# Optimization experiments

Measured on AMD Instinct MI355X. Metric: run time of the kernel, lower is better.

Reference implementation:

```python
import jax, jax.numpy as jnp
import numpy as np

B, S, D, M = 4, 2048, 1024, 4  # batch, seq_len, d_model, n_stride_masks


def setup_inputs() -> dict:
    key = jax.random.key(0)
    ks = jax.random.split(key, 10)
    lin = lambda k: jax.random.normal(k, (D, D), jnp.float32) / np.float32(np.sqrt(D))
    return {
        "x": jax.random.normal(ks[0], (B, S, D), jnp.float32),
        "stride_masks": jax.random.randint(ks[1], (M, S, S), 0, 2, jnp.int32),
        "Wq": lin(ks[2]), "bq": jnp.zeros((D,), jnp.float32),
        "Wk": lin(ks[3]), "bk": jnp.zeros((D,), jnp.float32),
        "Wv": lin(ks[4]), "bv": jnp.zeros((D,), jnp.float32),
        "Wo": lin(ks[5]), "bo": jnp.zeros((D,), jnp.float32),
    }


def reference(x, stride_masks, Wq, bq, Wk, bk, Wv, bv, Wo, bo):
    scale = jnp.float32(np.sqrt(D))
    Q = x @ Wq + bq  # [B,S,D]
    K = x @ Wk + bk
    V = x @ Wv + bv
    # scores are identical for every mask; compute once (same math as the loop)
    scores = jnp.einsum("bqd,bkd->bqk", Q, K) / scale  # [B,S,S]
    masked = jnp.where(stride_masks[:, None] == 0, jnp.float32(-1e9), scores[None])  # [M,B,S,S]
    weights = jax.nn.softmax(masked, axis=-1)
    # sum over masks then divide by M == mean(stack(outs), 0)
    out = jnp.einsum("mbqk,bkd->bqd", weights, V) / jnp.float32(M)
    return out @ Wo + bo
```

## Files before the change

kernel.cpp:

```cpp
#include <hip/hip_runtime.h>
#include <hip/hip_bf16.h>
#include <stdint.h>

#define B_ 4
#define S_ 2048
#define D_ 1024
#define M_ 4

typedef __bf16 bf16;
typedef _Float16 f16;
typedef unsigned char u8;
typedef __bf16 bf16x8 __attribute__((ext_vector_type(8)));
typedef _Float16 f16x8 __attribute__((ext_vector_type(8)));
typedef float f32x4 __attribute__((ext_vector_type(4)));

__device__ __forceinline__ void async_copy16(const void* g, void* l) {
  __builtin_amdgcn_global_load_lds(
      (const __attribute__((address_space(1))) void*)g,
      (__attribute__((address_space(3))) void*)l, 16, 0, 0);
}

__global__ __launch_bounds__(256) void prep(
    const float* __restrict__ x, const float* __restrict__ w0,
    const float* __restrict__ w1, const float* __restrict__ w2,
    const float* __restrict__ w3, const int* __restrict__ masks,
    bf16* __restrict__ xc, bf16* __restrict__ WT, u8* __restrict__ pk) {
  __shared__ bf16 t[64][65];
  const int blk = blockIdx.x;
  const int tid = threadIdx.x;
  const long SS = (long)S_ * S_;

  if (blk < 4096) {
    const long i = (long)blk * 2048 + tid * 8;
    const float4 a = *(const float4*)(x + i);
    const float4 b = *(const float4*)(x + i + 4);
    bf16x8 o;
    o[0] = (bf16)a.x; o[1] = (bf16)a.y; o[2] = (bf16)a.z; o[3] = (bf16)a.w;
    o[4] = (bf16)b.x; o[5] = (bf16)b.y; o[6] = (bf16)b.z; o[7] = (bf16)b.w;
    *(bf16x8*)(xc + i) = o;
  } else if (blk < 5120) {
    const int local = blk - 4096;
    const int z = local >> 8;
    const int rem = local & 255;
    const int r0 = (rem >> 4) * 64;
    const int c0 = (rem & 15) * 64;
    const int tx = tid & 63;
    const int ty = tid >> 6;
    const float* in = (z == 0) ? w0 : (z == 1) ? w1 : (z == 2) ? w2 : w3;
    bf16* out = WT + (long)z * D_ * D_;
    for (int i = ty; i < 64; i += 4)
      t[i][tx] = (bf16)in[(long)(r0 + i) * D_ + c0 + tx];
    __syncthreads();
    for (int i = ty; i < 64; i += 4)
      out[(long)(c0 + i) * D_ + r0 + tx] = t[tx][i];
  } else {
    const long e = (long)(blk - 5120) * 2048 + tid * 8;
    unsigned long long wv = 0;
#pragma unroll
    for (int m = 0; m < M_; ++m) {
      const int4 a = *(const int4*)(masks + m * SS + e);
      const int4 b = *(const int4*)(masks + m * SS + e + 4);
      const int v[8] = {a.x, a.y, a.z, a.w, b.x, b.y, b.z, b.w};
#pragma unroll
      for (int j = 0; j < 8; ++j)
        wv |= (unsigned long long)(v[j] != 0 ? 1u : 0u) << (8 * j + m);
    }
    *(unsigned long long*)(pk + e) = wv;
  }
}

__global__ __launch_bounds__(256) void transposeB(
    const bf16* __restrict__ in, bf16* __restrict__ out,
    int rows, int cols, long ib, long ob) {
  __shared__ bf16 t[64][65];
  in += (long)blockIdx.z * ib;
  out += (long)blockIdx.z * ob;
  const int r0 = blockIdx.y * 64;
  const int c0 = blockIdx.x * 64;
  const int tx = threadIdx.x & 63;
  const int ty = threadIdx.x >> 6;
#pragma unroll
  for (int i = ty; i < 64; i += 4) t[i][tx] = in[(long)(r0 + i) * cols + c0 + tx];
  __syncthreads();
#pragma unroll
  for (int i = ty; i < 64; i += 4) out[(long)(c0 + i) * rows + r0 + tx] = t[tx][i];
}

#define MODE_PLAIN 0
#define MODE_EXP 1
#define MODE_QKV 2

template <typename OutT, int MODE>
__global__ __launch_bounds__(256) void gemm_bt(
    const bf16* __restrict__ A, long aB, int lda,
    const bf16* __restrict__ Bt, long bB, int ldb,
    OutT* __restrict__ C, long cB, int ldc,
    const float* __restrict__ bias0, const float* __restrict__ bias1,
    const float* __restrict__ bias2, float alpha, int K) {
  __shared__ __align__(16) bf16 As[2][128 * 64];
  __shared__ __align__(16) bf16 Bs[2][128 * 64];
  const int tid = threadIdx.x;
  const int lane = tid & 63;
  const int w = tid >> 6;
  const int wm = w & 1;
  const int wn = w >> 1;
  A += (long)blockIdx.z * aB;
  Bt += (long)blockIdx.z * bB;
  if (MODE != MODE_QKV) C += (long)blockIdx.z * cB;

  const int gx = gridDim.x;
  const int pid = blockIdx.y * gx + blockIdx.x;
  const int gsz = 16 * gx;
  const int bym = (pid / gsz) * 16 + (pid % 16);
  const int bxm = (pid % gsz) / 16;

  const int row0 = bym * 128;
  const int col0 = bxm * 128;
  const int quad = lane >> 4;
  const int l15 = lane & 15;
  const int srow = lane >> 3;
  const int scol = (lane & 7) * 8;

  f32x4 acc[4][4];
#pragma unroll
  for (int i = 0; i < 4; ++i)
#pragma unroll
    for (int j = 0; j < 4; ++j) acc[i][j] = (f32x4){0.f, 0.f, 0.f, 0.f};

  const int nk = K >> 6;

#pragma unroll
  for (int c = 0; c < 4; ++c) {
    const int r = c * 32 + w * 8;
    async_copy16(A + (long)(row0 + r + srow) * lda + scol, &As[0][r * 64]);
    async_copy16(Bt + (long)(col0 + r + srow) * ldb + scol, &Bs[0][r * 64]);
  }

  for (int i = 0; i < nk; ++i) {
    const int cur = i & 1;
    __syncthreads();
    if (i + 1 < nk) {
      const int kt = (i + 1) << 6;
      const int nxt = cur ^ 1;
#pragma unroll
      for (int c = 0; c < 4; ++c) {
        const int r = c * 32 + w * 8;
        async_copy16(A + (long)(row0 + r + srow) * lda + kt + scol, &As[nxt][r * 64]);
        async_copy16(Bt + (long)(col0 + r + srow) * ldb + kt + scol, &Bs[nxt][r * 64]);
      }
    }
#pragma unroll
    for (int ks = 0; ks < 2; ++ks) {
      bf16x8 af[4], bf[4];
#pragma unroll
      for (int j = 0; j < 4; ++j) {
        af[j] = *(const bf16x8*)&As[cur][(wm * 64 + j * 16 + l15) * 64 + ks * 32 + quad * 8];
        bf[j] = *(const bf16x8*)&Bs[cur][(wn * 64 + j * 16 + l15) * 64 + ks * 32 + quad * 8];
      }
#pragma unroll
      for (int mi = 0; mi < 4; ++mi)
#pragma unroll
        for (int ni = 0; ni < 4; ++ni)
          acc[mi][ni] = __builtin_amdgcn_mfma_f32_16x16x32_bf16(af[mi], bf[ni], acc[mi][ni], 0, 0, 0);
    }
  }

  const int grp = (MODE == MODE_QKV) ? (bxm >> 3) : 0;
  const float* bias = (MODE == MODE_QKV)
                          ? (grp == 0 ? bias0 : grp == 1 ? bias1 : bias2)
                          : bias0;
  const long NX = (long)B_ * S_ * D_;

#pragma unroll
  for (int mi = 0; mi < 4; ++mi)
#pragma unroll
    for (int ni = 0; ni < 4; ++ni) {
      const int col = col0 + wn * 64 + ni * 16 + l15;
      const int lcol = col & (D_ - 1);
      const float bv = bias ? bias[MODE == MODE_QKV ? lcol : col] : 0.0f;
#pragma unroll
      for (int r = 0; r < 4; ++r) {
        const int row = row0 + wm * 64 + mi * 16 + quad * 4 + r;
        const float val = acc[mi][ni][r] * alpha + bv;
        if (MODE == MODE_EXP) {
          C[(long)row * ldc + col] = (OutT)__expf(val);
        } else if (MODE == MODE_QKV) {
          C[grp * NX + (long)row * D_ + lcol] = (OutT)val;
        } else {
          C[(long)row * ldc + col] = (OutT)val;
        }
      }
    }
}

__device__ __forceinline__ void stage_half(const bf16* __restrict__ G, int ld,
                                           int row_base, int kcol,
                                           bf16* region, int tid) {
  const int r = tid >> 2;
  const int c = ((tid & 3) ^ ((tid >> 3) & 3)) << 3;
  const bf16* g = G + (long)(row_base + r) * ld + kcol + c;
  bf16* dst = region + ((tid >> 6) << 9);
  async_copy16(g, dst);
  async_copy16(g + (long)128 * ld, dst + 4096);
}

template <typename OutT, int MODE>
__global__ __launch_bounds__(512) void gemm256(
    const bf16* __restrict__ A, long aB, int lda,
    const bf16* __restrict__ Bt, long bB, int ldb,
    OutT* __restrict__ C, long cB, int ldc,
    const float* __restrict__ bias0, const float* __restrict__ bias1,
    const float* __restrict__ bias2, float alpha, int K) {
  __shared__ __align__(16) bf16 As[2][2][256 * 32];
  __shared__ __align__(16) bf16 Bs[2][2][256 * 32];
  const int tid = threadIdx.x;
  const int lane = tid & 63;
  const int w = tid >> 6;
  const int wm = w & 1;
  const int wn = w >> 1;
  const int quad = lane >> 4;
  const int l15 = lane & 15;
  const int fse = (quad ^ ((l15 >> 1) & 3)) << 3;

  A += (long)blockIdx.z * aB;
  Bt += (long)blockIdx.z * bB;
  if (MODE != MODE_QKV) C += (long)blockIdx.z * cB;

  const int gx = gridDim.x;
  const int pid = blockIdx.y * gx + blockIdx.x;
  const int gsz = 8 * gx;
  const int bym = (pid / gsz) * 8 + (pid % 8);
  const int bxm = (pid % gsz) / 8;
  const int row0 = bym * 256;
  const int col0 = bxm * 256;

  f32x4 acc[8][4];
#pragma unroll
  for (int i = 0; i < 8; ++i)
#pragma unroll
    for (int j = 0; j < 4; ++j) acc[i][j] = (f32x4){0.f, 0.f, 0.f, 0.f};

  const int nk = K >> 6;

  stage_half(A, lda, row0, 0, &As[0][0][0], tid);
  stage_half(Bt, ldb, col0, 0, &Bs[0][0][0], tid);
  stage_half(A, lda, row0, 32, &As[0][1][0], tid);
  stage_half(Bt, ldb, col0, 32, &Bs[0][1][0], tid);
  if (nk > 1) {
    stage_half(A, lda, row0, 64, &As[1][0][0], tid);
    stage_half(Bt, ldb, col0, 64, &Bs[1][0][0], tid);
    asm volatile("s_waitcnt vmcnt(4)" ::: "memory");
  } else {
    asm volatile("s_waitcnt vmcnt(0)" ::: "memory");
  }
  __builtin_amdgcn_s_barrier();
  __builtin_amdgcn_sched_barrier(0);

  for (int t = 0; t < nk; ++t) {
    const int buf = t & 1;
    bf16x8 af[8], b0, b1;

#pragma unroll
    for (int m = 0; m < 8; ++m)
      af[m] = *(const bf16x8*)&As[buf][0][(wm * 128 + m * 16 + l15) * 32 + fse];
    b0 = *(const bf16x8*)&Bs[buf][0][(wn * 64 + l15) * 32 + fse];
    b1 = *(const bf16x8*)&Bs[buf][0][(wn * 64 + 16 + l15) * 32 + fse];
    if (t + 1 < nk)
      stage_half(A, lda, row0, ((t + 1) << 6) + 32, &As[buf ^ 1][1][0], tid);
    __builtin_amdgcn_s_setprio(1);
#pragma unroll
    for (int m = 0; m < 8; ++m) {
      acc[m][0] = __builtin_amdgcn_mfma_f32_16x16x32_bf16(af[m], b0, acc[m][0], 0, 0, 0);
      acc[m][1] = __builtin_amdgcn_mfma_f32_16x16x32_bf16(af[m], b1, acc[m][1], 0, 0, 0);
    }
    __builtin_amdgcn_s_setprio(0);
    __builtin_amdgcn_s_barrier();
    __builtin_amdgcn_sched_barrier(0);

    b0 = *(const bf16x8*)&Bs[buf][0][(wn * 64 + 32 + l15) * 32 + fse];
    b1 = *(const bf16x8*)&Bs[buf][0][(wn * 64 + 48 + l15) * 32 + fse];
    if (t + 1 < nk)
      stage_half(Bt, ldb, col0, ((t + 1) << 6) + 32, &Bs[buf ^ 1][1][0], tid);
    __builtin_amdgcn_s_setprio(1);
#pragma unroll
    for (int m = 0; m < 8; ++m) {
      acc[m][2] = __builtin_amdgcn_mfma_f32_16x16x32_bf16(af[m], b0, acc[m][2], 0, 0, 0);
      acc[m][3] = __builtin_amdgcn_mfma_f32_16x16x32_bf16(af[m], b1, acc[m][3], 0, 0, 0);
    }
    __builtin_amdgcn_s_setprio(0);
    __builtin_amdgcn_s_barrier();
    __builtin_amdgcn_sched_barrier(0);

#pragma unroll
    for (int m = 0; m < 8; ++m)
      af[m] = *(const bf16x8*)&As[buf][1][(wm * 128 + m * 16 + l15) * 32 + fse];
    b0 = *(const bf16x8*)&Bs[buf][1][(wn * 64 + l15) * 32 + fse];
    b1 = *(const bf16x8*)&Bs[buf][1][(wn * 64 + 16 + l15) * 32 + fse];
    if (t + 2 < nk)
      stage_half(A, lda, row0, (t + 2) << 6, &As[buf][0][0], tid);
    __builtin_amdgcn_s_setprio(1);
#pragma unroll
    for (int m = 0; m < 8; ++m) {
      acc[m][0] = __builtin_amdgcn_mfma_f32_16x16x32_bf16(af[m], b0, acc[m][0], 0, 0, 0);
      acc[m][1] = __builtin_amdgcn_mfma_f32_16x16x32_bf16(af[m], b1, acc[m][1], 0, 0, 0);
    }
    __builtin_amdgcn_s_setprio(0);
    __builtin_amdgcn_s_barrier();
    __builtin_amdgcn_sched_barrier(0);

    b0 = *(const bf16x8*)&Bs[buf][1][(wn * 64 + 32 + l15) * 32 + fse];
    b1 = *(const bf16x8*)&Bs[buf][1][(wn * 64 + 48 + l15) * 32 + fse];
    if (t + 2 < nk)
      stage_half(Bt, ldb, col0, (t + 2) << 6, &Bs[buf][0][0], tid);
    if (t + 2 < nk)
      asm volatile("s_waitcnt vmcnt(4)" ::: "memory");
    else
      asm volatile("s_waitcnt vmcnt(0)" ::: "memory");
    __builtin_amdgcn_s_setprio(1);
#pragma unroll
    for (int m = 0; m < 8; ++m) {
      acc[m][2] = __builtin_amdgcn_mfma_f32_16x16x32_bf16(af[m], b0, acc[m][2], 0, 0, 0);
      acc[m][3] = __builtin_amdgcn_mfma_f32_16x16x32_bf16(af[m], b1, acc[m][3], 0, 0, 0);
    }
    __builtin_amdgcn_s_setprio(0);
    __builtin_amdgcn_s_barrier();
    __builtin_amdgcn_sched_barrier(0);
  }

  const int grp = (MODE == MODE_QKV) ? (bxm >> 2) : 0;
  const float* bias = (MODE == MODE_QKV)
                          ? (grp == 0 ? bias0 : grp == 1 ? bias1 : bias2)
                          : bias0;
  const long NX = (long)B_ * S_ * D_;
#pragma unroll
  for (int mi = 0; mi < 8; ++mi)
#pragma unroll
    for (int ni = 0; ni < 4; ++ni) {
      const int col = col0 + wn * 64 + ni * 16 + l15;
      const int lcol = col & (D_ - 1);
      const float bv = bias ? bias[MODE == MODE_QKV ? lcol : col] : 0.0f;
#pragma unroll
      for (int r = 0; r < 4; ++r) {
        const int row = row0 + wm * 128 + mi * 16 + quad * 4 + r;
        const float val = acc[mi][ni][r] * alpha + bv;
        if (MODE == MODE_EXP) {
          C[(long)row * ldc + col] = (OutT)__expf(val);
        } else if (MODE == MODE_QKV) {
          C[grp * NX + (long)row * D_ + lcol] = (OutT)val;
        } else {
          C[(long)row * ldc + col] = (OutT)val;
        }
      }
    }
}

__global__ __launch_bounds__(256) void softmax_combine(
    const f16* __restrict__ E, const u8* __restrict__ pk, bf16* __restrict__ P) {
  const int q = blockIdx.x;
  const int b = blockIdx.y;
  const int tid = threadIdx.x;
  const int lane = tid & 63;
  const int wv = tid >> 6;
  __shared__ float4 red[4];

  float e[8];
  {
    const f16x8 h = *(const f16x8*)(E + ((long)b * S_ + q) * S_ + tid * 8);
#pragma unroll
    for (int j = 0; j < 8; ++j) e[j] = (float)h[j];
  }
  const unsigned long long mb =
      *(const unsigned long long*)(pk + (long)q * S_ + tid * 8);

  float4 s = {0.f, 0.f, 0.f, 0.f};
#pragma unroll
  for (int j = 0; j < 8; ++j) {
    const unsigned bits = (unsigned)(mb >> (8 * j)) & 0xF;
    const float ev = e[j];
    if (bits & 1) s.x += ev;
    if (bits & 2) s.y += ev;
    if (bits & 4) s.z += ev;
    if (bits & 8) s.w += ev;
  }
#pragma unroll
  for (int o = 32; o > 0; o >>= 1) {
    s.x += __shfl_xor(s.x, o, 64);
    s.y += __shfl_xor(s.y, o, 64);
    s.z += __shfl_xor(s.z, o, 64);
    s.w += __shfl_xor(s.w, o, 64);
  }
  if (lane == 0) red[wv] = s;
  __syncthreads();
  const float4 t0 = red[0], t1 = red[1], t2 = red[2], t3 = red[3];
  const float r0 = 0.25f / (t0.x + t1.x + t2.x + t3.x);
  const float r1 = 0.25f / (t0.y + t1.y + t2.y + t3.y);
  const float r2 = 0.25f / (t0.z + t1.z + t2.z + t3.z);
  const float r3 = 0.25f / (t0.w + t1.w + t2.w + t3.w);

  bf16x8 o;
#pragma unroll
  for (int j = 0; j < 8; ++j) {
    const unsigned bits = (unsigned)(mb >> (8 * j)) & 0xF;
    const float wgt = ((bits & 1) ? r0 : 0.f) + ((bits & 2) ? r1 : 0.f) +
                      ((bits & 4) ? r2 : 0.f) + ((bits & 8) ? r3 : 0.f);
    o[j] = (bf16)(e[j] * wgt);
  }
  *(bf16x8*)(P + ((long)b * S_ + q) * S_ + tid * 8) = o;
}

extern "C" void kernel_launch(void* const* d_in, const int* in_sizes, int n_in,
                              void* d_out, int out_size, void* d_ws, size_t ws_size,
                              hipStream_t stream) {
  const float* x = (const float*)d_in[0];
  const int* masks = (const int*)d_in[1];
  const float* bq = (const float*)d_in[3];
  const float* bk = (const float*)d_in[5];
  const float* bv = (const float*)d_in[7];
  const float* bo = (const float*)d_in[9];
  float* out = (float*)d_out;

  const long DD = (long)D_ * D_;
  const long SD = (long)S_ * D_;
  const long NX = (long)B_ * SD;
  const long SS = (long)S_ * S_;

  bf16* xc = (bf16*)d_ws;
  bf16* WqT = xc + NX;
  bf16* WoT = WqT + 3 * DD;
  u8* pk = (u8*)(WoT + DD);
  bf16* Q = (bf16*)(pk + SS);
  bf16* K = Q + NX;
  bf16* V = K + NX;
  bf16* VT = V + NX;
  bf16* P = VT + NX;
  f16* E = (f16*)(P + (long)B_ * SS);
  bf16* attn = Q;

  dim3 blk(256);
  dim3 blk512(512);

  prep<<<dim3(7168), blk, 0, stream>>>(
      x, (const float*)d_in[2], (const float*)d_in[4], (const float*)d_in[6],
      (const float*)d_in[8], masks, xc, WqT, pk);

  gemm256<bf16, MODE_QKV><<<dim3(12, 32), blk512, 0, stream>>>(
      xc, 0, D_, WqT, 0, D_, Q, 0, D_, bq, bk, bv, 1.0f, D_);

  transposeB<<<dim3(16, 32, B_), blk, 0, stream>>>(V, VT, S_, D_, SD, SD);

  gemm256<f16, MODE_EXP><<<dim3(8, 8, B_), blk512, 0, stream>>>(
      Q, SD, D_, K, SD, D_, E, SS, S_, nullptr, nullptr, nullptr, 1.0f / 32.0f, D_);

  softmax_combine<<<dim3(S_, B_), blk, 0, stream>>>(E, pk, P);

  gemm_bt<bf16, MODE_PLAIN><<<dim3(8, 16, B_), blk, 0, stream>>>(
      P, SS, S_, VT, SD, S_, attn, SD, D_, nullptr, nullptr, nullptr, 1.0f, S_);

  gemm_bt<float, MODE_PLAIN><<<dim3(8, 64), blk, 0, stream>>>(
      attn, 0, D_, WoT, 0, D_, out, 0, D_, bo, nullptr, nullptr, 1.0f, D_);
}
```

Before: 370.8 us.

## Replace gemm_bt with 256x128 half-K pipelined gemmA for QKV, PV and output projections

Adds a new 512-thread GEMM kernel with 256x128 tiles that splits each 64-wide K step into two 32-wide halves. Each half is staged asynchronously into swizzled LDS buffers under explicit vmcnt waits, raw barriers and raised wave priority around the MFMA block. It replaces the 128x128 gemm_bt used for P@V and the output projection, and the gemm256 used for the QKV projection. The aim is to overlap global loads with MFMA work and avoid LDS bank conflicts, at the cost of hand-counted waitcnt logic that must match the number of issued copies exactly.

```diff
diff --git a/kernel.cpp b/kernel.cpp
--- a/kernel.cpp
+++ b/kernel.cpp
@@ -89,37 +89,61 @@
 #define MODE_PLAIN 0
 #define MODE_EXP 1
 #define MODE_QKV 2
+#define MODE_PV 3
+
+__device__ __forceinline__ void stage128(const bf16* __restrict__ G, int ld,
+                                         int kcol, bf16* region, int tid) {
+  const int r = tid >> 2;
+  const int c = ((tid & 3) ^ ((tid >> 3) & 3)) << 3;
+  async_copy16(G + (long)r * ld + kcol + c, region + ((tid >> 6) << 9));
+}
+__device__ __forceinline__ void stage256(const bf16* __restrict__ G, int ld,
+                                         int kcol, bf16* region, int tid) {
+  const int r = tid >> 2;
+  const int c = ((tid & 3) ^ ((tid >> 3) & 3)) << 3;
+  const bf16* g = G + (long)r * ld + kcol + c;
+  bf16* dst = region + ((tid >> 6) << 9);
+  async_copy16(g, dst);
+  async_copy16(g + (long)128 * ld, dst + 4096);
+}
 
 template <typename OutT, int MODE>
-__global__ __launch_bounds__(256) void gemm_bt(
-    const bf16* __restrict__ A, long aB, int lda,
-    const bf16* __restrict__ Bt, long bB, int ldb,
-    OutT* __restrict__ C, long cB, int ldc,
+__global__ __launch_bounds__(512) void gemmA(
+    const bf16* __restrict__ A, int lda,
+    const bf16* __restrict__ Bt, long bzs, int ldb,
+    OutT* __restrict__ C, int ldc,
     const float* __restrict__ bias0, const float* __restrict__ bias1,
     const float* __restrict__ bias2, float alpha, int K) {
-  __shared__ __align__(16) bf16 As[2][128 * 64];
-  __shared__ __align__(16) bf16 Bs[2][128 * 64];
+  __shared__ __align__(16) bf16 As[2][2][256 * 32];
+  __shared__ __align__(16) bf16 Bs[2][2][128 * 32];
   const int tid = threadIdx.x;
   const int lane = tid & 63;
   const int w = tid >> 6;
-  const int wm = w & 1;
-  const int wn = w >> 1;
-  A += (long)blockIdx.z * aB;
-  Bt += (long)blockIdx.z * bB;
-  if (MODE != MODE_QKV) C += (long)blockIdx.z * cB;
+  const int wm = w & 3;
+  const int wn = w >> 2;
+  const int quad = lane >> 4;
+  const int l15 = lane & 15;
+  const int fse = (quad ^ ((l15 >> 1) & 3)) << 3;
 
   const int gx = gridDim.x;
   const int pid = blockIdx.y * gx + blockIdx.x;
-  const int gsz = 16 * gx;
-  const int bym = (pid / gsz) * 16 + (pid % 16);
-  const int bxm = (pid % gsz) / 16;
-
-  const int row0 = bym * 128;
+  const int gsz = 8 * gx;
+  const int bym = (pid / gsz) * 8 + (pid % 8);
+  const int bxm = (pid % gsz) / 8;
+  const int row0 = bym * 256;
   const int col0 = bxm * 128;
-  const int quad = lane >> 4;
-  const int l15 = lane & 15;
-  const int srow = lane >> 3;
-  const int scol = (lane & 7) * 8;
+
+  const bf16* Arow = A + (long)row0 * lda;
+  const bf16* Bcol;
+  int grp = 0;
+  if (MODE == MODE_QKV) {
+    grp = col0 >> 10;
+    Bcol = Bt + (long)grp * ((long)D_ * D_) + (long)(col0 & (D_ - 1)) * ldb;
+  } else if (MODE == MODE_PV) {
+    Bcol = Bt + (long)(row0 >> 11) * bzs + (long)col0 * ldb;
+  } else {
+    Bcol = Bt + (long)col0 * ldb;
+  }
 
   f32x4 acc[4][4];
 #pragma unroll
@@ -129,65 +153,89 @@
 
   const int nk = K >> 6;
 
-#pragma unroll
-  for (int c = 0; c < 4; ++c) {
-    const int r = c * 32 + w * 8;
-    async_copy16(A + (long)(row0 + r + srow) * lda + scol, &As[0][r * 64]);
-    async_copy16(Bt + (long)(col0 + r + srow) * ldb + scol, &Bs[0][r * 64]);
-  }
-
-  for (int i = 0; i < nk; ++i) {
-    const int cur = i & 1;
-    __syncthreads();
-    if (i + 1 < nk) {
-      const int kt = (i + 1) << 6;
-      const int nxt = cur ^ 1;
-#pragma unroll
-      for (int c = 0; c < 4; ++c) {
-        const int r = c * 32 + w * 8;
-        async_copy16(A + (long)(row0 + r + srow) * lda + kt + scol, &As[nxt][r * 64]);
-        async_copy16(Bt + (long)(col0 + r + srow) * ldb + kt + scol, &Bs[nxt][r * 64]);
-      }
-    }
-#pragma unroll
-    for (int ks = 0; ks < 2; ++ks) {
-      bf16x8 af[4], bf[4];
-#pragma unroll
-      for (int j = 0; j < 4; ++j) {
-        af[j] = *(const bf16x8*)&As[cur][(wm * 64 + j * 16 + l15) * 64 + ks * 32 + quad * 8];
-        bf[j] = *(const bf16x8*)&Bs[cur][(wn * 64 + j * 16 + l15) * 64 + ks * 32 + quad * 8];
-      }
-#pragma unroll
-      for (int mi = 0; mi < 4; ++mi)
-#pragma unroll
-        for (int ni = 0; ni < 4; ++ni)
-          acc[mi][ni] = __builtin_amdgcn_mfma_f32_16x16x32_bf16(af[mi], bf[ni], acc[mi][ni], 0, 0, 0);
-    }
-  }
-
-  const int grp = (MODE == MODE_QKV) ? (bxm >> 3) : 0;
+  stage256(Arow, lda, 0, &As[0][0][0], tid);
+  stage128(Bcol, ldb, 0, &Bs[0][0][0], tid);
+  stage256(Arow, lda, 32, &As[0][1][0], tid);
+  stage128(Bcol, ldb, 32, &Bs[0][1][0], tid);
+  stage256(Arow, lda, 64, &As[1][0][0], tid);
+  stage128(Bcol, ldb, 64, &Bs[1][0][0], tid);
+  asm volatile("s_waitcnt vmcnt(3)" ::: "memory");
+  __builtin_amdgcn_s_barrier();
+  __builtin_amdgcn_sched_barrier(0);
+
+  for (int t = 0; t < nk; ++t) {
+    const int buf = t & 1;
+    bf16x8 af[4], bf[4];
+
+#pragma unroll
+    for (int j = 0; j < 4; ++j) {
+      af[j] = *(const bf16x8*)&As[buf][0][(wm * 64 + j * 16 + l15) * 32 + fse];
+      bf[j] = *(const bf16x8*)&Bs[buf][0][(wn * 64 + j * 16 + l15) * 32 + fse];
+    }
+    if (t + 1 < nk) {
+      const int kt = ((t + 1) << 6) + 32;
+      stage256(Arow, lda, kt, &As[buf ^ 1][1][0], tid);
+      stage128(Bcol, ldb, kt, &Bs[buf ^ 1][1][0], tid);
+    }
+    __builtin_amdgcn_s_setprio(1);
+#pragma unroll
+    for (int mi = 0; mi < 4; ++mi)
+#pragma unroll
+      for (int ni = 0; ni < 4; ++ni)
+        acc[mi][ni] = __builtin_amdgcn_mfma_f32_16x16x32_bf16(af[mi], bf[ni], acc[mi][ni], 0, 0, 0);
+    __builtin_amdgcn_s_setprio(0);
+    if (t + 1 < nk)
+      asm volatile("s_waitcnt vmcnt(6)" ::: "memory");
+    else
+      asm volatile("s_waitcnt vmcnt(0)" ::: "memory");
+    __builtin_amdgcn_s_barrier();
+    __builtin_amdgcn_sched_barrier(0);
+
+#pragma unroll
+    for (int j = 0; j < 4; ++j) {
+      af[j] = *(const bf16x8*)&As[buf][1][(wm * 64 + j * 16 + l15) * 32 + fse];
+      bf[j] = *(const bf16x8*)&Bs[buf][1][(wn * 64 + j * 16 + l15) * 32 + fse];
+    }
+    if (t + 2 < nk) {
+      const int kt = (t + 2) << 6;
+      stage256(Arow, lda, kt, &As[buf][0][0], tid);
+      stage128(Bcol, ldb, kt, &Bs[buf][0][0], tid);
+    }
+    __builtin_amdgcn_s_setprio(1);
+#pragma unroll
+    for (int mi = 0; mi < 4; ++mi)
+#pragma unroll
+      for (int ni = 0; ni < 4; ++ni)
+        acc[mi][ni] = __builtin_amdgcn_mfma_f32_16x16x32_bf16(af[mi], bf[ni], acc[mi][ni], 0, 0, 0);
+    __builtin_amdgcn_s_setprio(0);
+    if (t + 2 < nk)
+      asm volatile("s_waitcnt vmcnt(6)" ::: "memory");
+    else if (t + 1 < nk)
+      asm volatile("s_waitcnt vmcnt(3)" ::: "memory");
+    __builtin_amdgcn_s_barrier();
+    __builtin_amdgcn_sched_barrier(0);
+  }
+
   const float* bias = (MODE == MODE_QKV)
                           ? (grp == 0 ? bias0 : grp == 1 ? bias1 : bias2)
                           : bias0;
   const long NX = (long)B_ * S_ * D_;
-
+  OutT* Cb = (MODE == MODE_QKV) ? C + (long)grp * NX : C;
 #pragma unroll
   for (int mi = 0; mi < 4; ++mi)
 #pragma unroll
     for (int ni = 0; ni < 4; ++ni) {
       const int col = col0 + wn * 64 + ni * 16 + l15;
-      const int lcol = col & (D_ - 1);
-      const float bv = bias ? bias[MODE == MODE_QKV ? lcol : col] : 0.0f;
+      const int ccol = (MODE == MODE_QKV) ? (col & (D_ - 1)) : col;
+      const float bv = bias ? bias[ccol] : 0.0f;
 #pragma unroll
       for (int r = 0; r < 4; ++r) {
         const int row = row0 + wm * 64 + mi * 16 + quad * 4 + r;
         const float val = acc[mi][ni][r] * alpha + bv;
-        if (MODE == MODE_EXP) {
-          C[(long)row * ldc + col] = (OutT)__expf(val);
-        } else if (MODE == MODE_QKV) {
-          C[grp * NX + (long)row * D_ + lcol] = (OutT)val;
+        if (MODE == MODE_QKV) {
+          Cb[(long)row * D_ + ccol] = (OutT)val;
         } else {
-          C[(long)row * ldc + col] = (OutT)val;
+          Cb[(long)row * ldc + col] = (OutT)val;
         }
       }
     }
@@ -443,8 +491,8 @@
       x, (const float*)d_in[2], (const float*)d_in[4], (const float*)d_in[6],
       (const float*)d_in[8], masks, xc, WqT, pk);
 
-  gemm256<bf16, MODE_QKV><<<dim3(12, 32), blk512, 0, stream>>>(
-      xc, 0, D_, WqT, 0, D_, Q, 0, D_, bq, bk, bv, 1.0f, D_);
+  gemmA<bf16, MODE_QKV><<<dim3(24, 32), blk512, 0, stream>>>(
+      xc, D_, WqT, 0, D_, Q, D_, bq, bk, bv, 1.0f, D_);
 
   transposeB<<<dim3(16, 32, B_), blk, 0, stream>>>(V, VT, S_, D_, SD, SD);
 
@@ -453,9 +501,9 @@
 
   softmax_combine<<<dim3(S_, B_), blk, 0, stream>>>(E, pk, P);
 
-  gemm_bt<bf16, MODE_PLAIN><<<dim3(8, 16, B_), blk, 0, stream>>>(
-      P, SS, S_, VT, SD, S_, attn, SD, D_, nullptr, nullptr, nullptr, 1.0f, S_);
-
-  gemm_bt<float, MODE_PLAIN><<<dim3(8, 64), blk, 0, stream>>>(
-      attn, 0, D_, WoT, 0, D_, out, 0, D_, bo, nullptr, nullptr, 1.0f, D_);
-}
+  gemmA<bf16, MODE_PV><<<dim3(8, 32), blk512, 0, stream>>>(
+      P, S_, VT, SD, S_, attn, D_, nullptr, nullptr, nullptr, 1.0f, S_);
+
+  gemmA<float, MODE_PLAIN><<<dim3(8, 32), blk512, 0, stream>>>(
+      attn, D_, WoT, 0, D_, out, D_, bo, nullptr, nullptr, 1.0f, D_);
+}
```

Result: faster. 357.9 us (median of 2 runs) (-3.5%).
